# Optimization experiments

Hardware: AMD Instinct MI355X
Metric: run time of the kernel (lower is better)

## Reference

```python
import jax, jax.numpy as jnp
import numpy as np

NUM_HEADS = 32
NUM_KV_HEADS = 8
HEAD_DIM = 128
SCALE = 1.0 / np.sqrt(HEAD_DIM)
LENGTHS = np.array([1024, 768, 512, 896], dtype=np.int32)  # ragged prefill lengths


def setup_inputs() -> dict:
    key = jax.random.key(0)
    kq, kk, kv = jax.random.split(key, 3)
    total = int(LENGTHS.sum())  # 3200
    q = jax.random.normal(kq, (total, NUM_HEADS * HEAD_DIM), dtype=jnp.float32)
    k = jax.random.normal(kk, (total, NUM_KV_HEADS * HEAD_DIM), dtype=jnp.float32)
    v = jax.random.normal(kv, (total, NUM_KV_HEADS * HEAD_DIM), dtype=jnp.float32)
    cu = jnp.asarray(np.concatenate([[0], np.cumsum(LENGTHS)]), dtype=jnp.int32)
    return {"q": q, "k": k, "v": v, "cu_seqlens": cu, "max_seqlen": 1024}


def _varlen_attn(q, k, v, cu_seqlens, max_seqlen):
    # q: [T, H*D], k/v: [T, KVH*D]; cu_seqlens: [B+1]
    T = q.shape[0]
    B = cu_seqlens.shape[0] - 1
    S = max_seqlen
    q = q.reshape(T, NUM_HEADS, HEAD_DIM)
    k = k.reshape(T, NUM_KV_HEADS, HEAD_DIM)
    v = v.reshape(T, NUM_KV_HEADS, HEAD_DIM)

    tok = jnp.arange(T, dtype=jnp.int32)
    batch_id = jnp.searchsorted(cu_seqlens[1:], tok, side="right").astype(jnp.int32)
    pos = tok - cu_seqlens[batch_id]

    # pad to [B, S, h, d] (zeros beyond each sequence, like _varlen_to_padded)
    qp = jnp.zeros((B, S, NUM_HEADS, HEAD_DIM), q.dtype).at[batch_id, pos].set(q)
    kp = jnp.zeros((B, S, NUM_KV_HEADS, HEAD_DIM), k.dtype).at[batch_id, pos].set(k)
    vp = jnp.zeros((B, S, NUM_KV_HEADS, HEAD_DIM), v.dtype).at[batch_id, pos].set(v)

    # GQA: repeat_interleave kv heads to match q heads
    rep = NUM_HEADS // NUM_KV_HEADS
    kp = jnp.repeat(kp, rep, axis=2)
    vp = jnp.repeat(vp, rep, axis=2)

    scores = jnp.einsum("bqhd,bkhd->bhqk", qp, kp) * SCALE
    # causal mask only (matches torch SDPA is_causal=True on padded input;
    # with equal q/k lengths, padded keys are never attended by valid queries)
    qi = jnp.arange(S)[:, None]
    kj = jnp.arange(S)[None, :]
    scores = jnp.where(kj <= qi, scores, jnp.finfo(scores.dtype).min)
    attn = jax.nn.softmax(scores, axis=-1)
    outp = jnp.einsum("bhqk,bkhd->bqhd", attn, vp)

    # unpad back to varlen and flatten heads
    out = outp[batch_id, pos]  # [T, H, D]
    return out.reshape(T, NUM_HEADS * HEAD_DIM)


def reference(q, k, v, cu_seqlens, max_seqlen):
    return _varlen_attn(q, k, v, cu_seqlens, max_seqlen)
```

## Files before the change

kernel.cpp:

```cpp
#include <hip/hip_runtime.h>
#include <hip/hip_bf16.h>

#define NH 32
#define NKVH 8
#define HD 128
#define KT 64
#define QT 32

typedef __attribute__((ext_vector_type(8))) __bf16 bf16x8;
typedef __attribute__((ext_vector_type(4))) __bf16 b16x4;
typedef __attribute__((ext_vector_type(4))) short s16x4;
typedef __attribute__((ext_vector_type(4))) float f32x4;
typedef __attribute__((ext_vector_type(2))) unsigned int u32x2;
typedef __attribute__((ext_vector_type(4))) unsigned int u32x4;

__device__ inline unsigned short f2bf(float f) {
    unsigned int u = __builtin_bit_cast(unsigned int, f);
    u += 0x7fffu + ((u >> 16) & 1u);
    return (unsigned short)(u >> 16);
}
__device__ inline unsigned int pk2(float lo, float hi) {
    return (unsigned int)f2bf(lo) | ((unsigned int)f2bf(hi) << 16);
}
__device__ inline f32x4 mfma16(bf16x8 a, bf16x8 b, f32x4 c) {
    return __builtin_amdgcn_mfma_f32_16x16x32_bf16(a, b, c, 0, 0, 0);
}
__device__ inline f32x4 mfma16k16(s16x4 a, s16x4 b, f32x4 c) {
#if __has_builtin(__builtin_amdgcn_mfma_f32_16x16x16bf16_1k)
    return __builtin_amdgcn_mfma_f32_16x16x16bf16_1k(a, b, c, 0, 0, 0);
#else
    f32x4 d = c;
    asm volatile("v_mfma_f32_16x16x16_bf16 %0, %1, %2, %0"
                 : "+v"(d) : "v"(a), "v"(b));
    return d;
#endif
}
__device__ inline void async16(unsigned short* lds, const unsigned short* g) {
    __builtin_amdgcn_global_load_lds(
        (const __attribute__((address_space(1))) unsigned int*)g,
        (__attribute__((address_space(3))) unsigned int*)lds, 16, 0, 0);
}
__device__ inline s16x4 pack4(f32x4 v) {
    b16x4 h = __builtin_convertvector(v, b16x4);
    return __builtin_bit_cast(s16x4, h);
}
__device__ inline bf16x8 pack8(f32x4 lo, f32x4 hi) {
    struct { s16x4 a, b; } t;
    t.a = pack4(lo);
    t.b = pack4(hi);
    return __builtin_bit_cast(bf16x8, t);
}

__global__ __launch_bounds__(256) void prep_kv(const float* __restrict__ kg,
                                               const float* __restrict__ vg,
                                               const int* __restrict__ cu,
                                               unsigned short* __restrict__ kb,
                                               unsigned short* __restrict__ vt,
                                               int* __restrict__ ctr) {
    const int b = blockIdx.y, kvh = blockIdx.z;
    if (blockIdx.x == 0 && b == 0 && kvh == 0 && threadIdx.x == 0) *ctr = 0;
    const int bstart = cu[b];
    const int L = cu[b + 1] - bstart;
    const int kv0 = blockIdx.x * 64;
    if (kv0 >= L) return;
    const int tid = threadIdx.x;
    const int wid = tid >> 6, lane = tid & 63;
    __shared__ __align__(16) unsigned short Vl[HD * 64];

    #pragma unroll
    for (int it = 0; it < 4; ++it) {
        int jp = wid * 8 + (lane >> 3);
        int c4 = (lane & 7) + it * 8;
        int j0 = jp * 2;
        int jj0 = kv0 + j0;
        f32x4 va = f32x4{0.f, 0.f, 0.f, 0.f}, vb = f32x4{0.f, 0.f, 0.f, 0.f};
        if (jj0 < L)     va = *(const f32x4*)&vg[(size_t)(bstart + jj0) * (NKVH * HD) + kvh * HD + c4 * 4];
        if (jj0 + 1 < L) vb = *(const f32x4*)&vg[(size_t)(bstart + jj0 + 1) * (NKVH * HD) + kvh * HD + c4 * 4];
        #pragma unroll
        for (int i = 0; i < 4; ++i) {
            int d = c4 * 4 + i;
            int idx = (d * 64 + j0) ^ ((d & 7) << 3);
            *(unsigned int*)&Vl[idx] = pk2(va[i], vb[i]);
        }
    }

    #pragma unroll
    for (int it = 0; it < 4; ++it) {
        int u = tid + it * 256;
        int j = u >> 4, c8 = u & 15;
        int jj = kv0 + j;
        if (jj < L) {
            const float* p = &kg[(size_t)(bstart + jj) * (NKVH * HD) + kvh * HD + c8 * 8];
            f32x4 a = *(const f32x4*)p;
            f32x4 bq = *(const f32x4*)(p + 4);
            u32x4 r = {pk2(a[0], a[1]), pk2(a[2], a[3]), pk2(bq[0], bq[1]), pk2(bq[2], bq[3])};
            *(u32x4*)&kb[(size_t)(bstart + jj) * (NKVH * HD) + kvh * HD + c8 * 8] = r;
        }
    }
    __syncthreads();

    const size_t vtb = (size_t)bstart * (NKVH * HD) + (size_t)kvh * HD * L;
    #pragma unroll
    for (int it = 0; it < 8; ++it) {
        int u = tid + it * 256;
        int d = u >> 4, c = u & 15;
        int j0 = c * 4;
        if (kv0 + j0 >= L) continue;
        int idx = d * 64 + (j0 ^ ((d & 7) << 3));
        u32x2 w = *(const u32x2*)&Vl[idx];
        *(u32x2*)&vt[vtb + (size_t)d * L + kv0 + j0] = w;
    }
}

__global__ __launch_bounds__(256, 2) void fa18(const float* __restrict__ qg,
                                               const unsigned short* __restrict__ kb,
                                               const unsigned short* __restrict__ vt,
                                               const int* __restrict__ cu,
                                               float* __restrict__ outg,
                                               int* __restrict__ ctr, int B) {
    const int tid = threadIdx.x;
    const int wid = tid >> 6, lane = tid & 63;
    const int lg = lane >> 4, lr = lane & 15;

    __shared__ __align__(16) unsigned short Klds[2][KT * HD];
    __shared__ __align__(16) unsigned short Vlds[2][HD * KT];
    __shared__ int s_item;

    int totalF = 0;
    {
        int prev = cu[0];
        #pragma unroll 1
        for (int bb = 0; bb < B; ++bb) {
            int nxt = cu[bb + 1];
            totalF += (nxt - prev + QT - 1) / QT;
            prev = nxt;
        }
    }
    const int totalItems = totalF * NKVH;
    const float scv = 0.08838834764831843f * 1.4426950408889634f;

    for (;;) {
        if (tid == 0) s_item = atomicAdd(ctr, 1);
        __syncthreads();
        const int item = s_item;
        if (item >= totalItems) return;

        const int kvh = item / totalF;
        const int f = item - kvh * totalF;
        int rem = f, bstart = 0, L = 0, nqf = 0, found = 0;
        int prev = cu[0];
        #pragma unroll 1
        for (int bb = 0; bb < B; ++bb) {
            int nxt = cu[bb + 1];
            int len = nxt - prev;
            int nq = (len + QT - 1) / QT;
            if (!found) {
                if (rem < nq) { bstart = prev; L = len; nqf = nq; found = 1; }
                else rem -= nq;
            }
            prev = nxt;
        }
        const int qt = nqf - 1 - rem;
        const int q0 = qt * QT;
        const int h = kvh * 4 + wid;

        bf16x8 qf0[4], qf1[4];
        #pragma unroll
        for (int kk = 0; kk < 4; ++kk) {
            int row0 = q0 + lr;
            int tok0 = bstart + (row0 < L ? row0 : L - 1);
            const float* p = &qg[(size_t)tok0 * (NH * HD) + h * HD + kk * 32 + lg * 8];
            f32x4 a = *(const f32x4*)p;
            f32x4 bq = *(const f32x4*)(p + 4);
            qf0[kk] = pack8(a * scv, bq * scv);
        }
        #pragma unroll
        for (int kk = 0; kk < 4; ++kk) {
            int row1 = q0 + 16 + lr;
            int tok1 = bstart + (row1 < L ? row1 : L - 1);
            const float* p = &qg[(size_t)tok1 * (NH * HD) + h * HD + kk * 32 + lg * 8];
            f32x4 a = *(const f32x4*)p;
            f32x4 bq = *(const f32x4*)(p + 4);
            qf1[kk] = pack8(a * scv, bq * scv);
        }

        f32x4 acc0[8], acc1[8];
        #pragma unroll
        for (int i = 0; i < 8; ++i) {
            acc0[i] = f32x4{0.f, 0.f, 0.f, 0.f};
            acc1[i] = f32x4{0.f, 0.f, 0.f, 0.f};
        }
        float lsum0 = 0.f, lsum1 = 0.f;

        const int ntiles = (q0 + QT + KT - 1) / KT;
        const unsigned short* kbase = kb + (size_t)bstart * (NKVH * HD) + kvh * HD;
        const unsigned short* vbase = vt + (size_t)bstart * (NKVH * HD) + (size_t)kvh * HD * L;

        auto STAGE = [&](int buf, int kv0) {
            unsigned short* Kd = Klds[buf];
            unsigned short* Vd = Vlds[buf];
            #pragma unroll
            for (int i = 0; i < 4; ++i) {
                int U = i * 256 + tid;
                int j = U >> 4, u = U & 15;
                int up = (u & 8) | ((u ^ j) & 7);
                int jj = kv0 + j; if (jj >= L) jj = L - 1;
                async16(Kd + (size_t)U * 8, kbase + (size_t)jj * (NKVH * HD) + up * 8);
            }
            #pragma unroll
            for (int i = 0; i < 4; ++i) {
                int U = i * 256 + tid;
                int d = U >> 3, u = U & 7;
                int up = u ^ (d & 7);
                int col = kv0 + up * 8;
                if (col > L - 8) col = L - 8;
                async16(Vd + (size_t)U * 8, vbase + (size_t)d * L + col);
            }
        };

        STAGE(0, 0);
        __syncthreads();

        for (int kt = 0; kt < ntiles; ++kt) {
            const int kv0 = kt * KT;
            const int buf = kt & 1;
            if (kt + 1 < ntiles) STAGE(buf ^ 1, kv0 + KT);

            const unsigned short* Kc = Klds[buf];
            const unsigned short* Vc = Vlds[buf];

            const int shi_raw = ((q0 + QT - 1 - kv0) >> 4) + 1;
            const int s_hi = shi_raw < 4 ? shi_raw : 4;
            const bool needmask = (kv0 + KT - 1) > q0;
            const int qpos0 = q0 + lr;
            const int qpos1 = q0 + 16 + lr;

            f32x4 st0[4], st1[4];
            __builtin_amdgcn_s_setprio(1);
            #pragma unroll
            for (int s = 0; s < 4; ++s) {
                if (s < s_hi) {
                    f32x4 a0 = f32x4{0.f, 0.f, 0.f, 0.f};
                    f32x4 a1 = f32x4{0.f, 0.f, 0.f, 0.f};
                    int row = s * 16 + lr;
                    #pragma unroll
                    for (int kk = 0; kk < 4; ++kk) {
                        int un = kk * 4 + lg;
                        int cs = ((un & 8) | ((un ^ row) & 7)) * 8;
                        bf16x8 kf = *(const bf16x8*)&Kc[row * HD + cs];
                        a0 = mfma16(kf, qf0[kk], a0);
                        a1 = mfma16(kf, qf1[kk], a1);
                    }
                    st0[s] = a0;
                    st1[s] = a1;
                }
            }
            __builtin_amdgcn_s_setprio(0);

            #pragma unroll
            for (int s = 0; s < 4; ++s) {
                if (s < s_hi) {
                    #pragma unroll
                    for (int r = 0; r < 4; ++r) {
                        int j = kv0 + s * 16 + lg * 4 + r;
                        float p0 = __builtin_amdgcn_exp2f(st0[s][r]);
                        float p1 = __builtin_amdgcn_exp2f(st1[s][r]);
                        p0 = (needmask && j > qpos0) ? 0.f : p0;
                        p1 = (needmask && j > qpos1) ? 0.f : p1;
                        st0[s][r] = p0;
                        st1[s][r] = p1;
                        lsum0 += p0;
                        lsum1 += p1;
                    }
                }
            }

            #pragma unroll
            for (int s = 0; s < 4; ++s) {
                if (s < s_hi) {
                    s16x4 pb0 = pack4(st0[s]);
                    s16x4 pb1 = pack4(st1[s]);
                    __builtin_amdgcn_s_setprio(1);
                    #pragma unroll
                    for (int dsb = 0; dsb < 8; ++dsb) {
                        int vrow = dsb * 16 + lr;
                        int c0 = (s * 16 + lg * 4) ^ ((vrow & 7) << 3);
                        s16x4 vf = *(const s16x4*)&Vc[vrow * 64 + c0];
                        acc0[dsb] = mfma16k16(vf, pb0, acc0[dsb]);
                        acc1[dsb] = mfma16k16(vf, pb1, acc1[dsb]);
                    }
                    __builtin_amdgcn_s_setprio(0);
                }
            }
            __syncthreads();
        }

        {
            float l = lsum0;
            l += __shfl_xor(l, 16);
            l += __shfl_xor(l, 32);
            int q = q0 + lr;
            if (q < L) {
                float inv = 1.0f / l;
                size_t base = (size_t)(bstart + q) * (NH * HD) + h * HD;
                #pragma unroll
                for (int dsb = 0; dsb < 8; ++dsb) {
                    f32x4 o = acc0[dsb] * inv;
                    *(f32x4*)&outg[base + dsb * 16 + lg * 4] = o;
                }
            }
        }
        {
            float l = lsum1;
            l += __shfl_xor(l, 16);
            l += __shfl_xor(l, 32);
            int q = q0 + 16 + lr;
            if (q < L) {
                float inv = 1.0f / l;
                size_t base = (size_t)(bstart + q) * (NH * HD) + h * HD;
                #pragma unroll
                for (int dsb = 0; dsb < 8; ++dsb) {
                    f32x4 o = acc1[dsb] * inv;
                    *(f32x4*)&outg[base + dsb * 16 + lg * 4] = o;
                }
            }
        }
    }
}

extern "C" void kernel_launch(void* const* d_in, const int* in_sizes, int n_in,
                              void* d_out, int out_size, void* d_ws, size_t ws_size,
                              hipStream_t stream) {
    const float* q = (const float*)d_in[0];
    const float* k = (const float*)d_in[1];
    const float* v = (const float*)d_in[2];
    const int* cu  = (const int*)d_in[3];
    int T = in_sizes[0] / (NH * HD);
    int B = in_sizes[3] - 1;

    unsigned short* kb = (unsigned short*)d_ws;
    unsigned short* vt = kb + (size_t)T * (NKVH * HD);
    int* ctr = (int*)(vt + (size_t)T * (NKVH * HD));

    dim3 gkv((T + 63) / 64, B, NKVH);
    prep_kv<<<gkv, 256, 0, stream>>>(k, v, cu, kb, vt, ctr);

    fa18<<<dim3(512), dim3(256), 0, stream>>>(q, kb, vt, cu, (float*)d_out, ctr, B);
}
```

Baseline: 86.55 us.

## Store K/V tiles in LDS in MFMA fragment order for linear reads

The V-transpose buffer written by the prep kernel now uses a [token/4][d][4] layout instead of [d][token]. The attention kernel's async staging places K and V into LDS already in per-lane MFMA operand order, so the inner loops read fragments with a plain lane-indexed address instead of XOR-swizzled row/column arithmetic. This removes per-iteration address computation and aims for conflict-free contiguous LDS reads. The cost is more scattered global gather patterns during staging, and the tail clamp on t4 assumes L is divisible by 4.

```diff
diff --git a/kernel.cpp b/kernel.cpp
--- a/kernel.cpp
+++ b/kernel.cpp
@@ -103,16 +103,16 @@
     #pragma unroll
     for (int it = 0; it < 8; ++it) {
         int u = tid + it * 256;
-        int d = u >> 4, c = u & 15;
-        int j0 = c * 4;
+        int d = u & 127, t4l = u >> 7;
+        int j0 = t4l * 4;
         if (kv0 + j0 >= L) continue;
         int idx = d * 64 + (j0 ^ ((d & 7) << 3));
         u32x2 w = *(const u32x2*)&Vl[idx];
-        *(u32x2*)&vt[vtb + (size_t)d * L + kv0 + j0] = w;
-    }
-}
-
-__global__ __launch_bounds__(256, 2) void fa18(const float* __restrict__ qg,
+        *(u32x2*)&vt[vtb + ((size_t)((kv0 >> 2) + t4l) * HD + d) * 4] = w;
+    }
+}
+
+__global__ __launch_bounds__(256, 2) void fa19(const float* __restrict__ qg,
                                                const unsigned short* __restrict__ kb,
                                                const unsigned short* __restrict__ vt,
                                                const int* __restrict__ cu,
@@ -195,26 +195,30 @@
         const int ntiles = (q0 + QT + KT - 1) / KT;
         const unsigned short* kbase = kb + (size_t)bstart * (NKVH * HD) + kvh * HD;
         const unsigned short* vbase = vt + (size_t)bstart * (NKVH * HD) + (size_t)kvh * HD * L;
+        const int t4m = (L >> 2) - 1;
 
         auto STAGE = [&](int buf, int kv0) {
             unsigned short* Kd = Klds[buf];
             unsigned short* Vd = Vlds[buf];
             #pragma unroll
             for (int i = 0; i < 4; ++i) {
-                int U = i * 256 + tid;
-                int j = U >> 4, u = U & 15;
-                int up = (u & 8) | ((u ^ j) & 7);
-                int jj = kv0 + j; if (jj >= L) jj = L - 1;
-                async16(Kd + (size_t)U * 8, kbase + (size_t)jj * (NKVH * HD) + up * 8);
+                int sl = i * 256 + tid;
+                int inst = sl >> 6, lam = sl & 63;
+                int s = inst >> 2, kk = inst & 3;
+                int jj = kv0 + s * 16 + (lam & 15);
+                if (jj >= L) jj = L - 1;
+                async16(Kd + (size_t)sl * 8,
+                        kbase + (size_t)jj * (NKVH * HD) + kk * 32 + (lam >> 4) * 8);
             }
             #pragma unroll
             for (int i = 0; i < 4; ++i) {
-                int U = i * 256 + tid;
-                int d = U >> 3, u = U & 7;
-                int up = u ^ (d & 7);
-                int col = kv0 + up * 8;
-                if (col > L - 8) col = L - 8;
-                async16(Vd + (size_t)U * 8, vbase + (size_t)d * L + col);
+                int sl = i * 256 + tid;
+                int inst = sl >> 5, m = sl & 31;
+                int s = inst >> 3, dsb = inst & 7;
+                int d0 = dsb * 16 + 2 * (m & 7);
+                int t4 = (kv0 >> 2) + s * 4 + (m >> 3);
+                if (t4 > t4m) t4 = t4m;
+                async16(Vd + (size_t)sl * 8, vbase + ((size_t)t4 * HD + d0) * 4);
             }
         };
 
@@ -242,12 +246,9 @@
                 if (s < s_hi) {
                     f32x4 a0 = f32x4{0.f, 0.f, 0.f, 0.f};
                     f32x4 a1 = f32x4{0.f, 0.f, 0.f, 0.f};
-                    int row = s * 16 + lr;
                     #pragma unroll
                     for (int kk = 0; kk < 4; ++kk) {
-                        int un = kk * 4 + lg;
-                        int cs = ((un & 8) | ((un ^ row) & 7)) * 8;
-                        bf16x8 kf = *(const bf16x8*)&Kc[row * HD + cs];
+                        bf16x8 kf = *(const bf16x8*)&Kc[(((s * 4 + kk) * 64) + lane) * 8];
                         a0 = mfma16(kf, qf0[kk], a0);
                         a1 = mfma16(kf, qf1[kk], a1);
                     }
@@ -283,9 +284,7 @@
                     __builtin_amdgcn_s_setprio(1);
                     #pragma unroll
                     for (int dsb = 0; dsb < 8; ++dsb) {
-                        int vrow = dsb * 16 + lr;
-                        int c0 = (s * 16 + lg * 4) ^ ((vrow & 7) << 3);
-                        s16x4 vf = *(const s16x4*)&Vc[vrow * 64 + c0];
+                        s16x4 vf = *(const s16x4*)&Vc[(((s * 8 + dsb) * 64) + lane) * 4];
                         acc0[dsb] = mfma16k16(vf, pb0, acc0[dsb]);
                         acc1[dsb] = mfma16k16(vf, pb1, acc1[dsb]);
                     }
@@ -345,5 +344,5 @@
     dim3 gkv((T + 63) / 64, B, NKVH);
     prep_kv<<<gkv, 256, 0, stream>>>(k, v, cu, kb, vt, ctr);
 
-    fa18<<<dim3(512), dim3(256), 0, stream>>>(q, kb, vt, cu, (float*)d_out, ctr, B);
-}
+    fa19<<<dim3(512), dim3(256), 0, stream>>>(q, kb, vt, cu, (float*)d_out, ctr, B);
+}
```

After: 89.97 us. +4.0%, slower.
